# Performance work log

Measured on AMD Instinct MI355X. Metric: run time of the kernel, lower is better.

Reference implementation:

```python
import jax, jax.numpy as jnp
import numpy as np

N = 8192
IN_F = 512
OUT_F = 64
ALPHA = 0.2  # LeakyReLU negative slope
NEG_INF = -9e15


def setup_inputs() -> dict:
    key = jax.random.key(0)
    k1, k2, k3, k4 = jax.random.split(key, 4)
    x = jax.random.normal(k1, (N, IN_F), dtype=jnp.float32)
    adj = jax.random.randint(k2, (N, N), 0, 2, dtype=jnp.int32)
    # xavier_uniform with gain=1.414
    def xavier(k, shape, gain=1.414):
        fan_in, fan_out = shape[0], shape[1]
        a = gain * np.sqrt(6.0 / (fan_in + fan_out))
        return jax.random.uniform(k, shape, jnp.float32, -a, a)
    W = xavier(k3, (IN_F, OUT_F))
    a = xavier(k4, (2 * OUT_F, 1))
    return {"x": x, "adj": adj, "W": W, "a": a}


def reference(x, adj, W, a):
    h = x @ W  # [N, F]
    f = W.shape[1]
    # e[i,j] = leakyrelu([h_i, h_j] @ a) = leakyrelu(h_i@a1 + h_j@a2)
    e1 = h @ a[:f, 0]   # [N]
    e2 = h @ a[f:, 0]   # [N]
    e = jax.nn.leaky_relu(e1[:, None] + e2[None, :], negative_slope=ALPHA)  # [N, N]
    scores = jnp.where(adj > 0, e, NEG_INF)
    attention = jax.nn.softmax(scores, axis=1)  # dropout p=0.0 -> identity
    h_prime = attention @ h  # [N, F]
    return jax.nn.elu(h_prime)  # concat=True
```

## Files before the change

kernel.cpp:

```cpp
#include <hip/hip_runtime.h>
#include <hip/hip_bf16.h>

#define NN 8192
#define KF 512
#define FF 64
#define GAT_ALPHA 0.2f
#define MSHIFT 20.0f

typedef __attribute__((ext_vector_type(8))) __bf16 bf16x8;
typedef __attribute__((ext_vector_type(4))) float f32x4;

__global__ __launch_bounds__(256) void gat_linear(
    const float* __restrict__ x, const float* __restrict__ W,
    const float* __restrict__ av, __hip_bfloat16* __restrict__ ht,
    float* __restrict__ e1, float* __restrict__ e2)
{
    __shared__ float xs[32][68];
    __shared__ float Ws[32][64];
    __shared__ float ep[2][64][17];

    const int t  = threadIdx.x;
    const int fq = t & 15;
    const int rq = t >> 4;
    const int i0 = blockIdx.x * 64;

    float acc[4][4] = {};

    for (int kt = 0; kt < KF; kt += 32) {
        {
            const int k = t & 31, r8 = t >> 5;
            #pragma unroll
            for (int m = 0; m < 8; ++m) {
                int r = r8 + 8 * m;
                xs[k][r] = x[(size_t)(i0 + r) * KF + kt + k];
            }
        }
        {
            const int fw = t & 63, kq = t >> 6;
            #pragma unroll
            for (int m = 0; m < 8; ++m) {
                int k2 = kq + 4 * m;
                Ws[k2][fw] = W[(size_t)(kt + k2) * FF + fw];
            }
        }
        __syncthreads();
        #pragma unroll
        for (int kk = 0; kk < 32; kk += 4) {
            #pragma unroll
            for (int i = 0; i < 4; ++i) {
                f32x4 xv = *(const f32x4*)&xs[kk + i][rq * 4];
                f32x4 wv = *(const f32x4*)&Ws[kk + i][fq * 4];
                #pragma unroll
                for (int u = 0; u < 4; ++u)
                    #pragma unroll
                    for (int v = 0; v < 4; ++v)
                        acc[u][v] += xv[u] * wv[v];
            }
        }
        __syncthreads();
    }

    #pragma unroll
    for (int v = 0; v < 4; ++v) {
        int f = fq * 4 + v;
        union { ushort4 q; __hip_bfloat16 h[4]; } pk;
        #pragma unroll
        for (int u = 0; u < 4; ++u) pk.h[u] = __float2bfloat16(acc[u][v]);
        *(ushort4*)&ht[(size_t)f * NN + i0 + rq * 4] = pk.q;
    }

    f32x4 a1v = *(const f32x4*)&av[fq * 4];
    f32x4 a2v = *(const f32x4*)&av[64 + fq * 4];
    #pragma unroll
    for (int u = 0; u < 4; ++u) {
        float s1 = 0.f, s2 = 0.f;
        #pragma unroll
        for (int v = 0; v < 4; ++v) {
            s1 += acc[u][v] * a1v[v];
            s2 += acc[u][v] * a2v[v];
        }
        ep[0][rq * 4 + u][fq] = s1;
        ep[1][rq * 4 + u][fq] = s2;
    }
    __syncthreads();
    if (t < 64) {
        float s1 = 0.f, s2 = 0.f;
        #pragma unroll
        for (int q = 0; q < 16; ++q) { s1 += ep[0][t][q]; s2 += ep[1][t][q]; }
        e1[i0 + t] = s1;
        e2[i0 + t] = s2;
    }
}

__global__ __launch_bounds__(256) void gat_attn(
    const int* __restrict__ adj, const __hip_bfloat16* __restrict__ ht,
    const float* __restrict__ e1, const float* __restrict__ e2,
    float* __restrict__ out)
{
    __shared__ __hip_bfloat16 ps[16][72];
    __shared__ float l_red[16];

    const int t    = threadIdx.x;
    const int ii   = t >> 4;
    const int jq   = t & 15;
    const int i0   = blockIdx.x * 16;
    const int lane = t & 63;
    const int wv   = t >> 6;
    const int n16  = lane & 15;
    const int quad = lane >> 4;

    const float e1i = e1[i0 + ii];
    float ms = e1i + MSHIFT;
    const float mi = ms > 0.f ? ms : GAT_ALPHA * ms;

    if (t < 16) l_red[t] = 0.f;

    const int*   arow = adj + (size_t)(i0 + ii) * NN + jq * 4;
    const float* e2p  = e2 + jq * 4;
    const __hip_bfloat16* htp = ht + (size_t)(wv * 16 + n16) * NN + quad * 8;
    const __hip_bfloat16* psa = &ps[n16][quad * 8];
    const __hip_bfloat16* psb = &ps[n16][32 + quad * 8];

    int4   a0 = *(const int4*)(arow);
    float4 v0 = *(const float4*)(e2p);
    int4   a1 = *(const int4*)(arow + 64);
    float4 v1 = *(const float4*)(e2p + 64);

    float lpart = 0.f;
    f32x4 dacc = {0.f, 0.f, 0.f, 0.f};

    __syncthreads();

#define GAT_TILE(AV, EV, TILE, PF_OFF)                                         \
    {                                                                          \
        int4 a_ = (AV); float4 e_ = (EV);                                      \
        if ((TILE) + (PF_OFF) < 128) {                                         \
            (AV) = *(const int4*)(arow + ((TILE) + (PF_OFF)) * 64);            \
            (EV) = *(const float4*)(e2p + ((TILE) + (PF_OFF)) * 64);           \
        }                                                                      \
        union { uint2 u; __hip_bfloat16 h[4]; } pk;                            \
        float s_, p_;                                                          \
        s_ = e1i + e_.x; s_ = s_ > 0.f ? s_ : GAT_ALPHA * s_;                  \
        p_ = (a_.x > 0) ? __expf(s_ - mi) : 0.f;                              \
        pk.h[0] = __float2bfloat16(p_); lpart += __bfloat162float(pk.h[0]);    \
        s_ = e1i + e_.y; s_ = s_ > 0.f ? s_ : GAT_ALPHA * s_;                  \
        p_ = (a_.y > 0) ? __expf(s_ - mi) : 0.f;                              \
        pk.h[1] = __float2bfloat16(p_); lpart += __bfloat162float(pk.h[1]);    \
        s_ = e1i + e_.z; s_ = s_ > 0.f ? s_ : GAT_ALPHA * s_;                  \
        p_ = (a_.z > 0) ? __expf(s_ - mi) : 0.f;                              \
        pk.h[2] = __float2bfloat16(p_); lpart += __bfloat162float(pk.h[2]);    \
        s_ = e1i + e_.w; s_ = s_ > 0.f ? s_ : GAT_ALPHA * s_;                  \
        p_ = (a_.w > 0) ? __expf(s_ - mi) : 0.f;                              \
        pk.h[3] = __float2bfloat16(p_); lpart += __bfloat162float(pk.h[3]);    \
        *(uint2*)&ps[ii][jq * 4] = pk.u;                                       \
        __syncthreads();                                                       \
        bf16x8 af0 = *(const bf16x8*)psa;                                      \
        bf16x8 af1 = *(const bf16x8*)psb;                                      \
        bf16x8 bf0 = *(const bf16x8*)(htp + (size_t)(TILE) * 64);              \
        bf16x8 bf1 = *(const bf16x8*)(htp + (size_t)(TILE) * 64 + 32);         \
        dacc = __builtin_amdgcn_mfma_f32_16x16x32_bf16(af0, bf0, dacc, 0, 0, 0);\
        dacc = __builtin_amdgcn_mfma_f32_16x16x32_bf16(af1, bf1, dacc, 0, 0, 0);\
        __syncthreads();                                                       \
    }

    for (int tile = 0; tile < 128; tile += 2) {
        GAT_TILE(a0, v0, tile, 2)
        GAT_TILE(a1, v1, tile + 1, 2)
    }
#undef GAT_TILE

    atomicAdd(&l_red[ii], lpart);
    __syncthreads();

    #pragma unroll
    for (int r = 0; r < 4; ++r) {
        int row = quad * 4 + r;
        float hv = dacc[r] / l_red[row];
        float o = hv > 0.f ? hv : __expf(hv) - 1.f;
        out[(size_t)(i0 + row) * FF + wv * 16 + n16] = o;
    }
}

extern "C" void kernel_launch(void* const* d_in, const int* in_sizes, int n_in,
                              void* d_out, int out_size, void* d_ws, size_t ws_size,
                              hipStream_t stream) {
    const float* x   = (const float*)d_in[0];
    const int*   adj = (const int*)d_in[1];
    const float* W   = (const float*)d_in[2];
    const float* av  = (const float*)d_in[3];
    float* out = (float*)d_out;

    char* wsb = (char*)d_ws;
    __hip_bfloat16* ht = (__hip_bfloat16*)wsb;
    float* e1 = (float*)(wsb + (1 << 20));
    float* e2 = e1 + NN;

    gat_linear<<<128, 256, 0, stream>>>(x, W, av, ht, e1, e2);
    gat_attn<<<512, 256, 0, stream>>>(adj, ht, e1, e2, out);
}
```

Before: 461.8 us.

## Process adjacency in 512-column chunks with double-buffered LDS and fewer barriers

The attention kernel now handles the adjacency row in 512-column chunks. It computes probabilities for the whole chunk into a double-buffered LDS tile and prefetches the next chunk's adjacency into registers, which leaves one barrier per chunk instead of two per 64 columns. The exp is replaced by a hardware exp2, with e1 and e2 prescaled by log2(e) in the linear kernel. The linear kernel is retiled to 32 rows per block so it launches twice as many blocks. The costs are higher register use from the eight int4 adjacency prefetches, a launch_bounds occupancy hint, and more LDS per block.

```diff
diff --git a/kernel.cpp b/kernel.cpp
--- a/kernel.cpp
+++ b/kernel.cpp
@@ -6,6 +6,13 @@
 #define FF 64
 #define GAT_ALPHA 0.2f
 #define MSHIFT 20.0f
+#define LOG2E 1.44269504f
+
+#define JCH 512
+#define NCH (NN / JCH)
+#define PST 520
+
+#define EXP2F(x) __builtin_amdgcn_exp2f(x)
 
 typedef __attribute__((ext_vector_type(8))) __bf16 bf16x8;
 typedef __attribute__((ext_vector_type(4))) float f32x4;
@@ -15,46 +22,37 @@
     const float* __restrict__ av, __hip_bfloat16* __restrict__ ht,
     float* __restrict__ e1, float* __restrict__ e2)
 {
-    __shared__ float xs[32][68];
+    __shared__ float xs[32][33];
     __shared__ float Ws[32][64];
-    __shared__ float ep[2][64][17];
+    __shared__ float ep[2][32][17];
 
     const int t  = threadIdx.x;
     const int fq = t & 15;
     const int rq = t >> 4;
-    const int i0 = blockIdx.x * 64;
+    const int i0 = blockIdx.x * 32;
 
-    float acc[4][4] = {};
+    const int kl = t & 31, r0 = t >> 5;
+    const int fw = t & 63, kq = t >> 6;
+
+    float acc[2][4] = {};
 
     for (int kt = 0; kt < KF; kt += 32) {
-        {
-            const int k = t & 31, r8 = t >> 5;
-            #pragma unroll
-            for (int m = 0; m < 8; ++m) {
-                int r = r8 + 8 * m;
-                xs[k][r] = x[(size_t)(i0 + r) * KF + kt + k];
-            }
-        }
-        {
-            const int fw = t & 63, kq = t >> 6;
-            #pragma unroll
-            for (int m = 0; m < 8; ++m) {
-                int k2 = kq + 4 * m;
-                Ws[k2][fw] = W[(size_t)(kt + k2) * FF + fw];
-            }
-        }
+        #pragma unroll
+        for (int m = 0; m < 4; ++m)
+            xs[kl][r0 + 8 * m] = x[(size_t)(i0 + r0 + 8 * m) * KF + kt + kl];
+        #pragma unroll
+        for (int m = 0; m < 8; ++m)
+            Ws[kq + 4 * m][fw] = W[(size_t)(kt + kq + 4 * m) * FF + fw];
         __syncthreads();
         #pragma unroll
-        for (int kk = 0; kk < 32; kk += 4) {
+        for (int kk = 0; kk < 32; ++kk) {
+            float x0 = xs[kk][rq * 2];
+            float x1 = xs[kk][rq * 2 + 1];
+            f32x4 wv = *(const f32x4*)&Ws[kk][fq * 4];
             #pragma unroll
-            for (int i = 0; i < 4; ++i) {
-                f32x4 xv = *(const f32x4*)&xs[kk + i][rq * 4];
-                f32x4 wv = *(const f32x4*)&Ws[kk + i][fq * 4];
-                #pragma unroll
-                for (int u = 0; u < 4; ++u)
-                    #pragma unroll
-                    for (int v = 0; v < 4; ++v)
-                        acc[u][v] += xv[u] * wv[v];
+            for (int v = 0; v < 4; ++v) {
+                acc[0][v] += x0 * wv[v];
+                acc[1][v] += x1 * wv[v];
             }
         }
         __syncthreads();
@@ -63,41 +61,41 @@
     #pragma unroll
     for (int v = 0; v < 4; ++v) {
         int f = fq * 4 + v;
-        union { ushort4 q; __hip_bfloat16 h[4]; } pk;
-        #pragma unroll
-        for (int u = 0; u < 4; ++u) pk.h[u] = __float2bfloat16(acc[u][v]);
-        *(ushort4*)&ht[(size_t)f * NN + i0 + rq * 4] = pk.q;
+        union { ushort2 q; __hip_bfloat16 h[2]; } pk;
+        pk.h[0] = __float2bfloat16(acc[0][v]);
+        pk.h[1] = __float2bfloat16(acc[1][v]);
+        *(ushort2*)&ht[(size_t)f * NN + i0 + rq * 2] = pk.q;
     }
 
     f32x4 a1v = *(const f32x4*)&av[fq * 4];
     f32x4 a2v = *(const f32x4*)&av[64 + fq * 4];
     #pragma unroll
-    for (int u = 0; u < 4; ++u) {
+    for (int u = 0; u < 2; ++u) {
         float s1 = 0.f, s2 = 0.f;
         #pragma unroll
         for (int v = 0; v < 4; ++v) {
             s1 += acc[u][v] * a1v[v];
             s2 += acc[u][v] * a2v[v];
         }
-        ep[0][rq * 4 + u][fq] = s1;
-        ep[1][rq * 4 + u][fq] = s2;
+        ep[0][rq * 2 + u][fq] = s1;
+        ep[1][rq * 2 + u][fq] = s2;
     }
     __syncthreads();
-    if (t < 64) {
+    if (t < 32) {
         float s1 = 0.f, s2 = 0.f;
         #pragma unroll
         for (int q = 0; q < 16; ++q) { s1 += ep[0][t][q]; s2 += ep[1][t][q]; }
-        e1[i0 + t] = s1;
-        e2[i0 + t] = s2;
+        e1[i0 + t] = s1 * LOG2E;
+        e2[i0 + t] = s2 * LOG2E;
     }
 }
 
-__global__ __launch_bounds__(256) void gat_attn(
+__global__ __launch_bounds__(256, 2) void gat_attn(
     const int* __restrict__ adj, const __hip_bfloat16* __restrict__ ht,
     const float* __restrict__ e1, const float* __restrict__ e2,
     float* __restrict__ out)
 {
-    __shared__ __hip_bfloat16 ps[16][72];
+    __shared__ __hip_bfloat16 ps[2][16][PST];
     __shared__ float l_red[16];
 
     const int t    = threadIdx.x;
@@ -109,65 +107,60 @@
     const int n16  = lane & 15;
     const int quad = lane >> 4;
 
-    const float e1i = e1[i0 + ii];
-    float ms = e1i + MSHIFT;
-    const float mi = ms > 0.f ? ms : GAT_ALPHA * ms;
+    const float e1L = e1[i0 + ii];
+    float ms = e1L + MSHIFT * LOG2E;
+    const float miL = ms > 0.f ? ms : GAT_ALPHA * ms;
 
     if (t < 16) l_red[t] = 0.f;
 
     const int*   arow = adj + (size_t)(i0 + ii) * NN + jq * 4;
     const float* e2p  = e2 + jq * 4;
-    const __hip_bfloat16* htp = ht + (size_t)(wv * 16 + n16) * NN + quad * 8;
-    const __hip_bfloat16* psa = &ps[n16][quad * 8];
-    const __hip_bfloat16* psb = &ps[n16][32 + quad * 8];
+    const __hip_bfloat16* hbase = ht + (size_t)(wv * 16 + n16) * NN + quad * 8;
 
-    int4   a0 = *(const int4*)(arow);
-    float4 v0 = *(const float4*)(e2p);
-    int4   a1 = *(const int4*)(arow + 64);
-    float4 v1 = *(const float4*)(e2p + 64);
+    int4 aj[8];
+    #pragma unroll
+    for (int g = 0; g < 8; ++g)
+        aj[g] = *(const int4*)(arow + g * 64);
 
     float lpart = 0.f;
     f32x4 dacc = {0.f, 0.f, 0.f, 0.f};
 
-    __syncthreads();
-
-#define GAT_TILE(AV, EV, TILE, PF_OFF)                                         \
-    {                                                                          \
-        int4 a_ = (AV); float4 e_ = (EV);                                      \
-        if ((TILE) + (PF_OFF) < 128) {                                         \
-            (AV) = *(const int4*)(arow + ((TILE) + (PF_OFF)) * 64);            \
-            (EV) = *(const float4*)(e2p + ((TILE) + (PF_OFF)) * 64);           \
-        }                                                                      \
-        union { uint2 u; __hip_bfloat16 h[4]; } pk;                            \
-        float s_, p_;                                                          \
-        s_ = e1i + e_.x; s_ = s_ > 0.f ? s_ : GAT_ALPHA * s_;                  \
-        p_ = (a_.x > 0) ? __expf(s_ - mi) : 0.f;                              \
-        pk.h[0] = __float2bfloat16(p_); lpart += __bfloat162float(pk.h[0]);    \
-        s_ = e1i + e_.y; s_ = s_ > 0.f ? s_ : GAT_ALPHA * s_;                  \
-        p_ = (a_.y > 0) ? __expf(s_ - mi) : 0.f;                              \
-        pk.h[1] = __float2bfloat16(p_); lpart += __bfloat162float(pk.h[1]);    \
-        s_ = e1i + e_.z; s_ = s_ > 0.f ? s_ : GAT_ALPHA * s_;                  \
-        p_ = (a_.z > 0) ? __expf(s_ - mi) : 0.f;                              \
-        pk.h[2] = __float2bfloat16(p_); lpart += __bfloat162float(pk.h[2]);    \
-        s_ = e1i + e_.w; s_ = s_ > 0.f ? s_ : GAT_ALPHA * s_;                  \
-        p_ = (a_.w > 0) ? __expf(s_ - mi) : 0.f;                              \
-        pk.h[3] = __float2bfloat16(p_); lpart += __bfloat162float(pk.h[3]);    \
-        *(uint2*)&ps[ii][jq * 4] = pk.u;                                       \
-        __syncthreads();                                                       \
-        bf16x8 af0 = *(const bf16x8*)psa;                                      \
-        bf16x8 af1 = *(const bf16x8*)psb;                                      \
-        bf16x8 bf0 = *(const bf16x8*)(htp + (size_t)(TILE) * 64);              \
-        bf16x8 bf1 = *(const bf16x8*)(htp + (size_t)(TILE) * 64 + 32);         \
-        dacc = __builtin_amdgcn_mfma_f32_16x16x32_bf16(af0, bf0, dacc, 0, 0, 0);\
-        dacc = __builtin_amdgcn_mfma_f32_16x16x32_bf16(af1, bf1, dacc, 0, 0, 0);\
-        __syncthreads();                                                       \
+    for (int c = 0; c < NCH; ++c) {
+        const int buf = c & 1;
+        #pragma unroll
+        for (int g = 0; g < 8; ++g) {
+            float4 e_ = *(const float4*)(e2p + c * JCH + g * 64);
+            int4   a_ = aj[g];
+            union { uint2 u; __hip_bfloat16 h[4]; } pk;
+            float s_, p_;
+            s_ = e1L + e_.x; s_ = s_ > 0.f ? s_ : GAT_ALPHA * s_;
+            p_ = a_.x > 0 ? EXP2F(s_ - miL) : 0.f;
+            pk.h[0] = __float2bfloat16(p_); lpart += __bfloat162float(pk.h[0]);
+            s_ = e1L + e_.y; s_ = s_ > 0.f ? s_ : GAT_ALPHA * s_;
+            p_ = a_.y > 0 ? EXP2F(s_ - miL) : 0.f;
+            pk.h[1] = __float2bfloat16(p_); lpart += __bfloat162float(pk.h[1]);
+            s_ = e1L + e_.z; s_ = s_ > 0.f ? s_ : GAT_ALPHA * s_;
+            p_ = a_.z > 0 ? EXP2F(s_ - miL) : 0.f;
+            pk.h[2] = __float2bfloat16(p_); lpart += __bfloat162float(pk.h[2]);
+            s_ = e1L + e_.w; s_ = s_ > 0.f ? s_ : GAT_ALPHA * s_;
+            p_ = a_.w > 0 ? EXP2F(s_ - miL) : 0.f;
+            pk.h[3] = __float2bfloat16(p_); lpart += __bfloat162float(pk.h[3]);
+            *(uint2*)&ps[buf][ii][g * 64 + jq * 4] = pk.u;
+        }
+        if (c + 1 < NCH) {
+            #pragma unroll
+            for (int g = 0; g < 8; ++g)
+                aj[g] = *(const int4*)(arow + (c + 1) * JCH + g * 64);
+        }
+        __syncthreads();
+        const __hip_bfloat16* hb = hbase + (size_t)c * JCH;
+        #pragma unroll
+        for (int kk = 0; kk < JCH / 32; ++kk) {
+            bf16x8 af = *(const bf16x8*)&ps[buf][n16][kk * 32 + quad * 8];
+            bf16x8 bf = *(const bf16x8*)(hb + kk * 32);
+            dacc = __builtin_amdgcn_mfma_f32_16x16x32_bf16(af, bf, dacc, 0, 0, 0);
+        }
     }
-
-    for (int tile = 0; tile < 128; tile += 2) {
-        GAT_TILE(a0, v0, tile, 2)
-        GAT_TILE(a1, v1, tile + 1, 2)
-    }
-#undef GAT_TILE
 
     atomicAdd(&l_red[ii], lpart);
     __syncthreads();
@@ -195,6 +188,6 @@
     float* e1 = (float*)(wsb + (1 << 20));
     float* e2 = e1 + NN;
 
-    gat_linear<<<128, 256, 0, stream>>>(x, W, av, ht, e1, e2);
+    gat_linear<<<256, 256, 0, stream>>>(x, W, av, ht, e1, e2);
     gat_attn<<<512, 256, 0, stream>>>(adj, ht, e1, e2, out);
 }
```

New measurement: 478.6 us. 1.04x slower.
